# Performance work log

Hardware: AMD Instinct MI355X
Metric: run time of the kernel (lower is better)

## Reference

```python
import jax, jax.numpy as jnp
import numpy as np

RADIUS = 0.2
K = 32  # num_neighbors


def setup_inputs() -> dict:
    key = jax.random.key(0)
    k1, k2, k3 = jax.random.split(key, 3)
    points_xyz = jax.random.uniform(k1, (2, 16384, 3), dtype=jnp.float32)
    center_xyz = jax.random.uniform(k2, (2, 2048, 3), dtype=jnp.float32)
    features = jax.random.normal(k3, (2, 64, 16384), dtype=jnp.float32)
    return {"points_xyz": points_xyz, "center_xyz": center_xyz, "features": features}


def _ball_query(center_xyz, points_xyz, k, radius):
    # squared distances (B, G, N) via ||c||^2 + ||p||^2 - 2 c.p (avoids (B,G,N,3) temp)
    c2 = jnp.sum(center_xyz * center_xyz, axis=-1)  # (B, G)
    p2 = jnp.sum(points_xyz * points_xyz, axis=-1)  # (B, N)
    cp = jnp.einsum('bgd,bnd->bgn', center_xyz, points_xyz)
    d2 = c2[:, :, None] + p2[:, None, :] - 2.0 * cp  # (B, G, N)
    n = points_xyz.shape[1]
    # key = point index if inside ball else sentinel N; first-K-in-ball == K smallest keys
    keys = jnp.where(d2 < radius * radius, jnp.arange(n, dtype=jnp.int32), n)
    neg_vals, _ = jax.lax.top_k(-keys, k)
    idx = -neg_vals  # (B, G, K) ascending point indices, sentinel n if <k found
    first = idx[..., :1]
    # pad missing slots with first found index (CUDA ball_query semantics), 0 if none
    idx = jnp.where(idx < n, idx, jnp.where(first < n, first, 0))
    return idx


def reference(points_xyz, center_xyz, features):
    idx = _ball_query(center_xyz, points_xyz, K, RADIUS)  # (B, G, K) int32
    gather = jax.vmap(lambda f, i: f[:, i])  # (C, N), (G, K) -> (C, G, K)
    grouped_xyz = gather(jnp.swapaxes(points_xyz, 1, 2), idx)  # (B, 3, G, K)
    # relative_xyz then normalize_xyz
    grouped_xyz = (grouped_xyz - jnp.swapaxes(center_xyz, 1, 2)[..., None]) / RADIUS
    grouped_features = gather(features, idx)  # (B, C, G, K)
    return grouped_xyz, grouped_features
```

## Files before the change

### kernel.cpp

```cpp
#include <hip/hip_runtime.h>
#include <hip/hip_bf16.h>

constexpr int NPTS = 16384;
constexpr int NCTR = 2048;
constexpr int NCH  = 64;
constexpr int KK   = 32;
constexpr int NB   = 2;
#define R2 0.04f

__global__ __launch_bounds__(256) void transpose_feats(
    const float* __restrict__ f, float* __restrict__ ft)
{
    __shared__ float tile[64][65];
    const int b  = blockIdx.y;
    const int n0 = blockIdx.x * 64;
    const int t  = threadIdx.x;
    const int nl = t & 63;
    const int q  = t >> 6;

    const float* fb = f + (size_t)b * NCH * NPTS;
#pragma unroll
    for (int r = 0; r < 16; ++r) {
        int c = r * 4 + q;
        tile[c][nl] = fb[(size_t)c * NPTS + n0 + nl];
    }
    __syncthreads();
    float* ftb = ft + ((size_t)b * NPTS + n0) * NCH;
#pragma unroll
    for (int r = 0; r < 16; ++r) {
        int n = r * 4 + q;
        ftb[(size_t)n * NCH + nl] = tile[nl][n];
    }
}

__global__ __launch_bounds__(256) void ballquery_group(
    const float* __restrict__ points,
    const float* __restrict__ centers,
    const float* __restrict__ feats,
    const float* __restrict__ featsT,
    float* __restrict__ out_xyz,
    float* __restrict__ out_feat)
{
#pragma clang fp contract(off)
    __shared__ int   s_idx[4][KK];
    __shared__ float s_f[4][KK][65];

    const int wave = threadIdx.x >> 6;
    const int lane = threadIdx.x & 63;
    const int cg   = blockIdx.x * 4 + wave;
    const int b    = cg >> 11;
    const int g    = cg & (NCTR - 1);

    const float* pb = points + (size_t)b * NPTS * 3;
    const float* cc = centers + (size_t)cg * 3;
    const float cx = cc[0], cy = cc[1], cz = cc[2];
    const float c2 = (cx * cx + cy * cy) + cz * cz;

    int* idxs = s_idx[wave];

    float x[8], y[8], z[8], nx[8], ny[8], nz[8];
#pragma unroll
    for (int j = 0; j < 8; ++j) {
        const int i = j * 64 + lane;
        x[j] = pb[i * 3 + 0]; y[j] = pb[i * 3 + 1]; z[j] = pb[i * 3 + 2];
    }
    int cnt = 0;
    for (int base = 0; base < NPTS; base += 512) {
        const int nb = (base + 512 < NPTS) ? base + 512 : 0;
#pragma unroll
        for (int j = 0; j < 8; ++j) {
            const int i = nb + j * 64 + lane;
            nx[j] = pb[i * 3 + 0]; ny[j] = pb[i * 3 + 1]; nz[j] = pb[i * 3 + 2];
        }
#pragma unroll
        for (int j = 0; j < 8; ++j) {
            const float p2 = (x[j] * x[j] + y[j] * y[j]) + z[j] * z[j];
            const float cp = (cx * x[j] + cy * y[j]) + cz * z[j];
            const float d2 = (c2 + p2) - 2.0f * cp;
            const bool hit = d2 < R2;
            const unsigned long long m = __ballot(hit);
            if (hit) {
                const int slot = cnt + __popcll(m & ((1ull << lane) - 1ull));
                if (slot < KK) idxs[slot] = base + j * 64 + lane;
            }
            cnt += (int)__popcll(m);
        }
        if (cnt >= KK) break;
#pragma unroll
        for (int j = 0; j < 8; ++j) { x[j] = nx[j]; y[j] = ny[j]; z[j] = nz[j]; }
    }
    __syncthreads();

    const int cpd = cnt < KK ? cnt : KK;
    const int first = (cnt > 0) ? idxs[0] : 0;
    if (lane < KK) {
        idxs[lane] = (lane < cpd) ? idxs[lane] : first;
    }
    __syncthreads();

    if (lane < KK) {
        const int id = idxs[lane];
        const float px = pb[id * 3 + 0];
        const float py = pb[id * 3 + 1];
        const float pz = pb[id * 3 + 2];
        const size_t ob = (((size_t)b * 3 + 0) * NCTR + g) * KK + lane;
        out_xyz[ob + (size_t)0 * NCTR * KK] = (px - cx) / 0.2f;
        out_xyz[ob + (size_t)1 * NCTR * KK] = (py - cy) / 0.2f;
        out_xyz[ob + (size_t)2 * NCTR * KK] = (pz - cz) / 0.2f;
    }

    float (*sf)[65] = s_f[wave];
    if (featsT) {
        const float* ftb = featsT + (size_t)b * NPTS * NCH;
#pragma unroll 8
        for (int k = 0; k < KK; ++k) {
            const int id = idxs[k];
            sf[k][lane] = ftb[(size_t)id * NCH + lane];
        }
    } else {
        const float* fb = feats + (size_t)b * NCH * NPTS;
        for (int k = 0; k < KK; ++k) {
            const int id = idxs[k];
            sf[k][lane] = fb[(size_t)lane * NPTS + id];
        }
    }
    __syncthreads();

    const int k  = lane & 31;
    const int ch = lane >> 5;
    const size_t ob = ((size_t)b * NCH * NCTR + g) * KK;
#pragma unroll
    for (int cc2 = 0; cc2 < 32; ++cc2) {
        const int c = cc2 * 2 + ch;
        out_feat[ob + (size_t)c * NCTR * KK + k] = sf[k][c];
    }
}

extern "C" void kernel_launch(void* const* d_in, const int* in_sizes, int n_in,
                              void* d_out, int out_size, void* d_ws, size_t ws_size,
                              hipStream_t stream) {
    const float* points  = (const float*)d_in[0];
    const float* centers = (const float*)d_in[1];
    const float* feats   = (const float*)d_in[2];

    float* out      = (float*)d_out;
    float* out_xyz  = out;
    float* out_feat = out + (size_t)NB * 3 * NCTR * KK;

    const size_t ftBytes = (size_t)NB * NPTS * NCH * sizeof(float);
    float* featsT = nullptr;
    if (ws_size >= ftBytes) {
        featsT = (float*)d_ws;
        transpose_feats<<<dim3(NPTS / 64, NB), 256, 0, stream>>>(feats, featsT);
    }

    ballquery_group<<<(NB * NCTR) / 4, 256, 0, stream>>>(
        points, centers, feats, featsT, out_xyz, out_feat);
}
```

Before: 88.28 us.

## Merge transpose with ball query and split feature gather into a separate kernel

The feature transpose and the ball query now run as disjoint block ranges of a single prep kernel, so they can execute concurrently instead of one after the other. The ball query writes neighbor indices to a workspace buffer. A new kernel gathers the grouped features with one block per center, using float4 loads and stores through a padded shared tile. This adds a kernel launch and an index round-trip through global memory in exchange for more overlap and wider memory accesses. The fallback path drops the software-pipelined point prefetch.

```diff
diff --git a/kernel.cpp b/kernel.cpp
--- a/kernel.cpp
+++ b/kernel.cpp
@@ -8,46 +8,44 @@
 constexpr int NB   = 2;
 #define R2 0.04f
 
-__global__ __launch_bounds__(256) void transpose_feats(
-    const float* __restrict__ f, float* __restrict__ ft)
-{
-    __shared__ float tile[64][65];
-    const int b  = blockIdx.y;
-    const int n0 = blockIdx.x * 64;
-    const int t  = threadIdx.x;
-    const int nl = t & 63;
-    const int q  = t >> 6;
-
-    const float* fb = f + (size_t)b * NCH * NPTS;
-#pragma unroll
-    for (int r = 0; r < 16; ++r) {
-        int c = r * 4 + q;
-        tile[c][nl] = fb[(size_t)c * NPTS + n0 + nl];
-    }
-    __syncthreads();
-    float* ftb = ft + ((size_t)b * NPTS + n0) * NCH;
-#pragma unroll
-    for (int r = 0; r < 16; ++r) {
-        int n = r * 4 + q;
-        ftb[(size_t)n * NCH + nl] = tile[nl][n];
-    }
-}
-
-__global__ __launch_bounds__(256) void ballquery_group(
+__global__ __launch_bounds__(256) void prep_kernel(
     const float* __restrict__ points,
     const float* __restrict__ centers,
     const float* __restrict__ feats,
-    const float* __restrict__ featsT,
+    float* __restrict__ featsT,
     float* __restrict__ out_xyz,
-    float* __restrict__ out_feat)
+    int* __restrict__ idx_out)
 {
 #pragma clang fp contract(off)
+    __shared__ float tile[64][65];
     __shared__ int   s_idx[4][KK];
-    __shared__ float s_f[4][KK][65];
+
+    if (blockIdx.x < 512) {
+        const int b  = blockIdx.x >> 8;
+        const int n0 = (blockIdx.x & 255) * 64;
+        const int t  = threadIdx.x;
+        const int nl = t & 63;
+        const int q  = t >> 6;
+
+        const float* fb = feats + (size_t)b * NCH * NPTS;
+#pragma unroll
+        for (int r = 0; r < 16; ++r) {
+            int c = r * 4 + q;
+            tile[c][nl] = fb[(size_t)c * NPTS + n0 + nl];
+        }
+        __syncthreads();
+        float* ftb = featsT + ((size_t)b * NPTS + n0) * NCH;
+#pragma unroll
+        for (int r = 0; r < 16; ++r) {
+            int n = r * 4 + q;
+            ftb[(size_t)n * NCH + nl] = tile[nl][n];
+        }
+        return;
+    }
 
     const int wave = threadIdx.x >> 6;
     const int lane = threadIdx.x & 63;
-    const int cg   = blockIdx.x * 4 + wave;
+    const int cg   = (blockIdx.x - 512) * 4 + wave;
     const int b    = cg >> 11;
     const int g    = cg & (NCTR - 1);
 
@@ -66,10 +64,10 @@
     }
     int cnt = 0;
     for (int base = 0; base < NPTS; base += 512) {
-        const int nb = (base + 512 < NPTS) ? base + 512 : 0;
+        const int nbb = (base + 512 < NPTS) ? base + 512 : 0;
 #pragma unroll
         for (int j = 0; j < 8; ++j) {
-            const int i = nb + j * 64 + lane;
+            const int i = nbb + j * 64 + lane;
             nx[j] = pb[i * 3 + 0]; ny[j] = pb[i * 3 + 1]; nz[j] = pb[i * 3 + 2];
         }
 #pragma unroll
@@ -94,12 +92,8 @@
     const int cpd = cnt < KK ? cnt : KK;
     const int first = (cnt > 0) ? idxs[0] : 0;
     if (lane < KK) {
-        idxs[lane] = (lane < cpd) ? idxs[lane] : first;
-    }
-    __syncthreads();
-
-    if (lane < KK) {
-        const int id = idxs[lane];
+        const int id = (lane < cpd) ? idxs[lane] : first;
+        idx_out[cg * KK + lane] = id;
         const float px = pb[id * 3 + 0];
         const float py = pb[id * 3 + 1];
         const float pz = pb[id * 3 + 2];
@@ -108,26 +102,103 @@
         out_xyz[ob + (size_t)1 * NCTR * KK] = (py - cy) / 0.2f;
         out_xyz[ob + (size_t)2 * NCTR * KK] = (pz - cz) / 0.2f;
     }
-
+}
+
+__global__ __launch_bounds__(256) void group_feats(
+    const float* __restrict__ featsT,
+    const int* __restrict__ idx_in,
+    float* __restrict__ out_feat)
+{
+    __shared__ float sf[KK][68];
+    __shared__ int   ids[KK];
+
+    const int t  = threadIdx.x;
+    const int cg = blockIdx.x;
+    const int b  = cg >> 11;
+    const int g  = cg & (NCTR - 1);
+
+    if (t < KK) ids[t] = idx_in[cg * KK + t];
+    __syncthreads();
+
+    const int wave = t >> 6, lane = t & 63;
+    const int li = lane & 15, r = lane >> 4;
+    const float* ftb = featsT + (size_t)b * NPTS * NCH;
+#pragma unroll
+    for (int i = 0; i < 2; ++i) {
+        const int k = wave * 8 + i * 4 + r;
+        const float4 v = *((const float4*)(ftb + (size_t)ids[k] * NCH) + li);
+        *(float4*)&sf[k][4 * li] = v;
+    }
+    __syncthreads();
+
+    const int kq = t & 7;
+    const int cL = t >> 3;
+    const size_t ob = ((size_t)b * NCH * NCTR + g) * KK;
+#pragma unroll
+    for (int p = 0; p < 2; ++p) {
+        const int c = cL + 32 * p;
+        float4 v;
+        v.x = sf[4 * kq + 0][c];
+        v.y = sf[4 * kq + 1][c];
+        v.z = sf[4 * kq + 2][c];
+        v.w = sf[4 * kq + 3][c];
+        *(float4*)(out_feat + ob + (size_t)c * NCTR * KK + 4 * kq) = v;
+    }
+}
+
+__global__ __launch_bounds__(256) void ballquery_group(
+    const float* __restrict__ points, const float* __restrict__ centers,
+    const float* __restrict__ feats, float* __restrict__ out_xyz,
+    float* __restrict__ out_feat)
+{
+#pragma clang fp contract(off)
+    __shared__ int   s_idx[4][KK];
+    __shared__ float s_f[4][KK][65];
+    const int wave = threadIdx.x >> 6, lane = threadIdx.x & 63;
+    const int cg = blockIdx.x * 4 + wave;
+    const int b = cg >> 11, g = cg & (NCTR - 1);
+    const float* pb = points + (size_t)b * NPTS * 3;
+    const float* cc = centers + (size_t)cg * 3;
+    const float cx = cc[0], cy = cc[1], cz = cc[2];
+    const float c2 = (cx * cx + cy * cy) + cz * cz;
+    int* idxs = s_idx[wave];
+    int cnt = 0;
+    for (int base = 0; base < NPTS; base += 64) {
+        const int i = base + lane;
+        const float px = pb[i * 3 + 0], py = pb[i * 3 + 1], pz = pb[i * 3 + 2];
+        const float p2 = (px * px + py * py) + pz * pz;
+        const float cp = (cx * px + cy * py) + cz * pz;
+        const float d2 = (c2 + p2) - 2.0f * cp;
+        const bool hit = d2 < R2;
+        const unsigned long long m = __ballot(hit);
+        if (hit) {
+            const int slot = cnt + __popcll(m & ((1ull << lane) - 1ull));
+            if (slot < KK) idxs[slot] = i;
+        }
+        cnt += (int)__popcll(m);
+        if (cnt >= KK) break;
+    }
+    __syncthreads();
+    const int cpd = cnt < KK ? cnt : KK;
+    const int first = (cnt > 0) ? idxs[0] : 0;
+    if (lane < KK) idxs[lane] = (lane < cpd) ? idxs[lane] : first;
+    __syncthreads();
+    if (lane < KK) {
+        const int id = idxs[lane];
+        const float px = pb[id * 3 + 0], py = pb[id * 3 + 1], pz = pb[id * 3 + 2];
+        const size_t ob = (((size_t)b * 3 + 0) * NCTR + g) * KK + lane;
+        out_xyz[ob + (size_t)0 * NCTR * KK] = (px - cx) / 0.2f;
+        out_xyz[ob + (size_t)1 * NCTR * KK] = (py - cy) / 0.2f;
+        out_xyz[ob + (size_t)2 * NCTR * KK] = (pz - cz) / 0.2f;
+    }
     float (*sf)[65] = s_f[wave];
-    if (featsT) {
-        const float* ftb = featsT + (size_t)b * NPTS * NCH;
-#pragma unroll 8
-        for (int k = 0; k < KK; ++k) {
-            const int id = idxs[k];
-            sf[k][lane] = ftb[(size_t)id * NCH + lane];
-        }
-    } else {
-        const float* fb = feats + (size_t)b * NCH * NPTS;
-        for (int k = 0; k < KK; ++k) {
-            const int id = idxs[k];
-            sf[k][lane] = fb[(size_t)lane * NPTS + id];
-        }
-    }
-    __syncthreads();
-
-    const int k  = lane & 31;
-    const int ch = lane >> 5;
+    const float* fb = feats + (size_t)b * NCH * NPTS;
+    for (int k = 0; k < KK; ++k) {
+        const int id = idxs[k];
+        sf[k][lane] = fb[(size_t)lane * NPTS + id];
+    }
+    __syncthreads();
+    const int k = lane & 31, ch = lane >> 5;
     const size_t ob = ((size_t)b * NCH * NCTR + g) * KK;
 #pragma unroll
     for (int cc2 = 0; cc2 < 32; ++cc2) {
@@ -147,13 +218,17 @@
     float* out_xyz  = out;
     float* out_feat = out + (size_t)NB * 3 * NCTR * KK;
 
-    const size_t ftBytes = (size_t)NB * NPTS * NCH * sizeof(float);
-    float* featsT = nullptr;
-    if (ws_size >= ftBytes) {
-        featsT = (float*)d_ws;
-        transpose_feats<<<dim3(NPTS / 64, NB), 256, 0, stream>>>(feats, featsT);
-    }
-
-    ballquery_group<<<(NB * NCTR) / 4, 256, 0, stream>>>(
-        points, centers, feats, featsT, out_xyz, out_feat);
-}
+    const size_t ftBytes  = (size_t)NB * NPTS * NCH * sizeof(float);
+    const size_t idxBytes = (size_t)NB * NCTR * KK * sizeof(int);
+
+    if (ws_size >= ftBytes + idxBytes) {
+        float* featsT = (float*)d_ws;
+        int*   idxbuf = (int*)((char*)d_ws + ftBytes);
+        prep_kernel<<<1536, 256, 0, stream>>>(points, centers, feats,
+                                              featsT, out_xyz, idxbuf);
+        group_feats<<<NB * NCTR, 256, 0, stream>>>(featsT, idxbuf, out_feat);
+    } else {
+        ballquery_group<<<(NB * NCTR) / 4, 256, 0, stream>>>(
+            points, centers, feats, out_xyz, out_feat);
+    }
+}
```

Result: slower. 91.28 us (+3.4%).
